# Optimization experiments

Measured on AMD Instinct MI355X. Metric: run time of the kernel, lower is better.

## Reference

```python
import jax, jax.numpy as jnp
import numpy as np

N, E, B, F, H = 100000, 800000, 128, 128, 128
G = 5
INV_BN = np.float32(1.0 / np.sqrt(1.0 + 1e-5))  # eval BatchNorm, running_mean=0, running_var=1

_HEAD_SHAPES = [("norm_emb_g", (2*H,)), ("norm_emb_b", (2*H,)),
                ("fc1_W", (16, 2*H+1)), ("fc1_b", (16,)),
                ("bn1_g", (16,)), ("bn1_b", (16,)),
                ("fc2_W", (2, 2*H+3)), ("fc2_b", (2,)),
                ("fc3a_W", (4, 2*H+5)), ("fc3a_b", (4,)),
                ("fc3b_W", (5, 2*H+5)), ("fc3b_b", (5,)),
                ("normc_g", (2*H+5,)), ("normc_b", (2*H+5,))]


def setup_inputs() -> dict:
    key = jax.random.key(0)
    ks = jax.random.split(key, 64)
    p = lambda i, shape: jax.random.normal(ks[i], shape, jnp.float32) * 0.05
    inp = {
        "x": jax.random.normal(ks[0], (N, F), jnp.float32),
        "edge_index": jax.random.randint(ks[1], (2, E), 0, N, dtype=jnp.int32),
        "edge_direction": jax.random.randint(ks[2], (E,), 0, 2, dtype=jnp.int32),
        "batch": jnp.sort(jax.random.randint(ks[3], (N,), 0, B, dtype=jnp.int32)),
        "graph_feature": jax.random.normal(ks[4], (B, G), jnp.float32),
        "task": 1,
    }
    i = 5
    for pref in ("pre", "suc"):
        for l in range(3):
            inp[pref + "_Wl%d" % l] = p(i, (H, H)); i += 1
            inp[pref + "_bl%d" % l] = p(i, (H,)); i += 1
            inp[pref + "_Wr%d" % l] = p(i, (H, H)); i += 1
    for name, shape in _HEAD_SHAPES:
        inp[name] = p(i, shape); i += 1
    return inp


def reference(x, edge_index, edge_direction, batch, graph_feature, task,
              pre_Wl0, pre_bl0, pre_Wr0, pre_Wl1, pre_bl1, pre_Wr1, pre_Wl2, pre_bl2, pre_Wr2,
              suc_Wl0, suc_bl0, suc_Wr0, suc_Wl1, suc_bl1, suc_Wr1, suc_Wl2, suc_bl2, suc_Wr2,
              norm_emb_g, norm_emb_b, fc1_W, fc1_b, bn1_g, bn1_b, fc2_W, fc2_b,
              fc3a_W, fc3a_b, fc3b_W, fc3b_b, normc_g, normc_b):
    src, dst = edge_index[0], edge_index[1]
    pre_mask = (edge_direction == 0).astype(x.dtype)
    suc_mask = (edge_direction == 1).astype(x.dtype)

    def sage(h, mask, Wl, bl, Wr):
        # PyG SAGEConv: lin_l(scatter_mean(x[src] -> dst)) + lin_r(h); masked edges emulate
        # the edge_direction slicing without data-dependent shapes.
        msg = h[src] * mask[:, None]                              # [E, H]
        agg = jax.ops.segment_sum(msg, dst, num_segments=N)      # [N, H]
        cnt = jax.ops.segment_sum(mask, dst, num_segments=N)     # [N]
        mean = agg / jnp.maximum(cnt, 1.0)[:, None]
        return mean @ Wl.T + bl + h @ Wr.T

    bn = lambda v, g, b: g * (v * INV_BN) + b  # eval-mode BatchNorm1d after reset

    pre_x, suc_x = x, x
    for Wl, bl, Wr in ((pre_Wl0, pre_bl0, pre_Wr0), (pre_Wl1, pre_bl1, pre_Wr1), (pre_Wl2, pre_bl2, pre_Wr2)):
        pre_x = jax.nn.relu(sage(pre_x, pre_mask, Wl, bl, Wr))
    for Wl, bl, Wr in ((suc_Wl0, suc_bl0, suc_Wr0), (suc_Wl1, suc_bl1, suc_Wr1), (suc_Wl2, suc_bl2, suc_Wr2)):
        suc_x = jax.nn.relu(sage(suc_x, suc_mask, Wl, bl, Wr))

    comb = jnp.concatenate([pre_x, suc_x], axis=1)               # [N, 2H]
    gsum = jax.ops.segment_sum(comb, batch, num_segments=B)
    gcnt = jax.ops.segment_sum(jnp.ones((N,), comb.dtype), batch, num_segments=B)
    combined = bn(gsum / jnp.maximum(gcnt, 1.0)[:, None], norm_emb_g, norm_emb_b)  # [B, 2H]

    lev_lsb = graph_feature[:, -1:]
    nx3 = graph_feature[:, -3:]
    out1 = bn(jax.nn.relu(jnp.concatenate([combined, lev_lsb], 1) @ fc1_W.T + fc1_b), bn1_g, bn1_b)
    out2 = jax.nn.relu(jnp.concatenate([combined, nx3], 1) @ fc2_W.T + fc2_b)
    pred = jnp.argmax(out2, axis=1)

    wf1 = graph_feature[:, 2:3]
    wf2 = graph_feature[:, 1:2]
    x3 = bn(jnp.concatenate([combined, wf1, wf2, nx3], 1), normc_g, normc_b)
    b1 = x3 @ fc3a_W.T + fc3a_b                                  # [B, 4]
    b2 = x3 @ fc3b_W.T + fc3b_b                                  # [B, 5]
    out3 = jnp.concatenate([jnp.where((pred == 0)[:, None], b1, 0.0),
                            jnp.where((pred == 1)[:, None], b2, 0.0)], axis=1)  # [B, 9]
    return (out1, out2, out3)
```

## Files before the change

kernel.cpp:

```cpp
#include <hip/hip_runtime.h>

constexpr int kN = 100000;
constexpr int kNpad = 100096;
constexpr int kE = 800000;
constexpr int kB = 128;
constexpr int kBinsPerDir = 391;
constexpr int kNB = 782;
constexpr int kRep = 64;
constexpr int kCtrs = kNB * kRep;
constexpr int kTiles = kNpad / 256;
constexpr float kInvBN = 0.99999500003749968f;

constexpr int kXconvBlocks = kNpad * 128 / 4 / 256;
constexpr int kWprepBlocks = 768;
constexpr int kBincountBlocks = (kE + 255) / 256;
constexpr int kGstartBlocks = (kN + 255) / 256;
constexpr int kPrepBlocks = kXconvBlocks + kWprepBlocks + kBincountBlocks + kGstartBlocks;

typedef short s16x8 __attribute__((ext_vector_type(8)));
typedef float f32x4 __attribute__((ext_vector_type(4)));

__device__ inline ushort bf16rne(float f) {
  uint u = __builtin_bit_cast(uint, f);
  u += 0x7fffu + ((u >> 16) & 1u);
  return (ushort)(u >> 16);
}
__device__ inline float bflo(uint v) { return __builtin_bit_cast(float, v << 16); }
__device__ inline float bfhi(uint v) { return __builtin_bit_cast(float, v & 0xffff0000u); }
__device__ inline uint pack2(float a, float b) {
  return (uint)bf16rne(a) | ((uint)bf16rne(b) << 16);
}

struct WPtrs { const float* Wl[6]; const float* Wr[6]; };


__global__ __launch_bounds__(256) void prep_kernel(
    const float* __restrict__ x, ushort* __restrict__ xb,
    WPtrs p, ushort* __restrict__ Wb,
    const int* __restrict__ ei, const int* __restrict__ ed,
    int* __restrict__ bincnt,
    const int* __restrict__ batch, int* __restrict__ gstart) {
  int bi = blockIdx.x;
  int t = threadIdx.x;
  if (bi < kXconvBlocks) {
    int i4 = (bi * 256 + t) * 4;
    ushort4 r;
    if (i4 < kN * 128) {
      float4 v = *(const float4*)&x[i4];
      r.x = bf16rne(v.x); r.y = bf16rne(v.y); r.z = bf16rne(v.z); r.w = bf16rne(v.w);
    } else {
      r.x = r.y = r.z = r.w = 0;
    }
    *(ushort4*)&xb[i4] = r;
  } else if (bi < kXconvBlocks + kWprepBlocks) {
    int id = (bi - kXconvBlocks) * 256 + t;
    int L = id >> 15;
    int o = (id >> 8) & 127, k = id & 255;
    const float* src = (k < 128) ? p.Wl[L] : p.Wr[L];
    Wb[id] = bf16rne(src[o * 128 + (k & 127)]);
  } else if (bi < kXconvBlocks + kWprepBlocks + kBincountBlocks) {
    int e = (bi - kXconvBlocks - kWprepBlocks) * 256 + t;
    if (e < kE) {
      int dst = ei[kE + e];
      int ctr = ((ed[e] * kBinsPerDir + (dst >> 8)) << 6) | ((e >> 8) & 63);
      atomicAdd(&bincnt[ctr], 1);
    }
  } else {
    int n = (bi - kXconvBlocks - kWprepBlocks - kBincountBlocks) * 256 + t;
    if (n < kN) {
      int b = batch[n];
      int bprev = (n == 0) ? -1 : batch[n - 1];
      for (int g = bprev + 1; g <= b; ++g) gstart[g] = n;
      if (n == kN - 1)
        for (int g = b + 1; g <= kB; ++g) gstart[g] = kN;
    }
  }
}


__global__ __launch_bounds__(256) void scan1_kernel(const int* __restrict__ in,
                                                    int* __restrict__ out,
                                                    int* __restrict__ bsum, int M) {
  __shared__ int s[256];
  int t = threadIdx.x;
  int idx = blockIdx.x * 1024 + t * 4;
  int4 v = {0, 0, 0, 0};
  if (idx < M) v = *(const int4*)&in[idx];
  int tsum = v.x + v.y + v.z + v.w;
  s[t] = tsum;
  __syncthreads();
  for (int d = 1; d < 256; d <<= 1) {
    int tmp = (t >= d) ? s[t - d] : 0;
    __syncthreads();
    s[t] += tmp;
    __syncthreads();
  }
  int excl = s[t] - tsum;
  if (idx < M) {
    int4 o;
    o.x = excl; o.y = excl + v.x; o.z = o.y + v.y; o.w = o.z + v.z;
    *(int4*)&out[idx] = o;
  }
  if (t == 255) bsum[blockIdx.x] = s[255];
}

__global__ __launch_bounds__(256) void scan2_kernel(int* __restrict__ bsum, int nb,
                                                    int* __restrict__ ghist) {
  __shared__ int s[256];
  int t = threadIdx.x;
  if (t < 128) ghist[t] = 0;
  int v = (t < nb) ? bsum[t] : 0;
  s[t] = v;
  __syncthreads();
  for (int d = 1; d < 256; d <<= 1) {
    int tmp = (t >= d) ? s[t - d] : 0;
    __syncthreads();
    s[t] += tmp;
    __syncthreads();
  }
  if (t < nb) bsum[t] = s[t] - v;
}

__global__ __launch_bounds__(256) void scan3_kernel(int* __restrict__ out,
                                                    const int* __restrict__ bsum, int M,
                                                    int* __restrict__ bincur) {
  int idx = blockIdx.x * 1024 + threadIdx.x * 4;
  int add = bsum[blockIdx.x];
  if (idx < M) {
    int4 o = *(int4*)&out[idx];
    o.x += add; o.y += add; o.z += add; o.w += add;
    *(int4*)&out[idx] = o;
    int4 z = {0, 0, 0, 0};
    *(int4*)&bincur[idx] = z;
  }
}


__global__ __launch_bounds__(256) void binscatter_kernel(const int* __restrict__ ei,
                                                         const int* __restrict__ ed,
                                                         const int* __restrict__ binoff,
                                                         int* __restrict__ bincur,
                                                         uint* __restrict__ binbuf,
                                                         float* __restrict__ comb_raw) {
  int gid = blockIdx.x * 256 + threadIdx.x;
  if (gid < kB * 256 / 4) {
    float4 z = {0.f, 0.f, 0.f, 0.f};
    *(float4*)&comb_raw[gid * 4] = z;
  }
  if (gid >= kE) return;
  int dst = ei[kE + gid];
  int ctr = ((ed[gid] * kBinsPerDir + (dst >> 8)) << 6) | ((gid >> 8) & 63);
  int pos = atomicAdd(&bincur[ctr], 1);
  binbuf[binoff[ctr] + pos] = (uint)ei[gid] | ((uint)(dst & 255) << 17);
}

__global__ __launch_bounds__(256) void binfill_kernel(const uint* __restrict__ binbuf,
                                                      const int* __restrict__ binoff,
                                                      int* __restrict__ csr,
                                                      int* __restrict__ cnt,
                                                      int* __restrict__ off,
                                                      int* __restrict__ ghist,
                                                      int* __restrict__ blockbase,
                                                      uint* __restrict__ perm) {
  __shared__ int lcnt[256];
  __shared__ int ls[256];
  __shared__ int lpos[256];
  int b = blockIdx.x;
  int t = threadIdx.x;
  perm[b * 256 + t] = (uint)kN;
  int dir = (b >= kBinsPerDir) ? 1 : 0;
  int nodeBase = (b - dir * kBinsPerDir) << 8;
  int e0 = binoff[b * kRep];
  int e1 = (b == kNB - 1) ? kE : binoff[(b + 1) * kRep];
  lcnt[t] = 0;
  __syncthreads();
  for (int e = e0 + t; e < e1; e += 256) atomicAdd(&lcnt[binbuf[e] >> 17], 1);
  __syncthreads();
  int my = lcnt[t];
  ls[t] = my;
  __syncthreads();
  for (int d = 1; d < 256; d <<= 1) {
    int tmp = (t >= d) ? ls[t - d] : 0;
    __syncthreads();
    ls[t] += tmp;
    __syncthreads();
  }
  int excl = ls[t] - my;
  lpos[t] = e0 + excl;
  int node = nodeBase + t;
  if (node < kN) {
    int g = dir * kN + node;
    cnt[g] = my;
    off[g] = e0 + excl;
  }
  if (t < 64) lcnt[t] = 0;
  __syncthreads();
  if (node < kN) atomicAdd(&lcnt[min(my, 63)], 1);
  __syncthreads();
  if (t < 64) blockbase[b * 64 + t] = atomicAdd(&ghist[dir * 64 + t], lcnt[t]);
  __syncthreads();
  for (int e = e0 + t; e < e1; e += 256) {
    uint v = binbuf[e];
    int pos = atomicAdd(&lpos[v >> 17], 1);
    csr[pos] = (int)(v & 0x1FFFFu);
  }
}


__global__ __launch_bounds__(64) void dscan_kernel(int* __restrict__ ghist) {
  __shared__ int s[64];
  int t = threadIdx.x;
  for (int dir = 0; dir < 2; ++dir) {
    int v = ghist[dir * 64 + t];
    s[t] = v;
    __syncthreads();
    for (int d = 1; d < 64; d <<= 1) {
      int tmp = (t >= d) ? s[t - d] : 0;
      __syncthreads();
      s[t] += tmp;
      __syncthreads();
    }
    ghist[dir * 64 + t] = s[t] - v;
    __syncthreads();
  }
}

__global__ __launch_bounds__(256) void dscatter_kernel(const int* __restrict__ cnt,
                                                       const int* __restrict__ ghist,
                                                       const int* __restrict__ blockbase,
                                                       uint* __restrict__ perm) {
  __shared__ int h[64];
  int b = blockIdx.x;
  int t = threadIdx.x;
  int dir = (b >= kBinsPerDir) ? 1 : 0;
  int node = (b - dir * kBinsPerDir) * 256 + t;
  if (t < 64) h[t] = 0;
  __syncthreads();
  if (node < kN) {
    int bucket = min(cnt[dir * kN + node], 63);
    int r = atomicAdd(&h[bucket], 1);
    int pos = ghist[dir * 64 + bucket] + blockbase[b * 64 + bucket] + r;
    int ch = pos >> 4, wi = pos & 15;
    int q = ch / 391, rr = ch - q * 391;
    int pos2 = ((rr * 16 + q) << 4) | wi;
    perm[dir * kNpad + pos2] = (uint)node;
  }
}


__global__ __launch_bounds__(1024) void fused_layer_kernel(
    const ushort* __restrict__ hin0, const ushort* __restrict__ hin1,
    ushort* __restrict__ hout0, ushort* __restrict__ hout1,
    const ushort* __restrict__ Wb0, const ushort* __restrict__ Wb1,
    const float* __restrict__ bl0, const float* __restrict__ bl1,
    const int* __restrict__ off, const int* __restrict__ cnt,
    const int* __restrict__ csr, const uint* __restrict__ perm) {
  __shared__ ushort Wlds[128 * 256];

  const int dir = (blockIdx.x >= kTiles) ? 1 : 0;
  const int tile = blockIdx.x - dir * kTiles;
  const ushort* __restrict__ h = dir ? hin1 : hin0;
  ushort* __restrict__ outp = dir ? hout1 : hout0;
  const ushort* __restrict__ Wb = dir ? Wb1 : Wb0;
  const float* __restrict__ bl = dir ? bl1 : bl0;
  const uint* __restrict__ pp = perm + (size_t)dir * kNpad;
  const int dirbase = dir * kN;

  const int t = threadIdx.x;
  const int w = t >> 6;
  const int l = t & 63;
  const int lr = l & 15;
  const int lq = l >> 4;
  const int swz = lr & 7;

  const int node = (int)pp[tile * 256 + w * 16 + lr];
  int s = 0, c = 0;
  if (node < kN) {
    int bkt = dirbase + node;
    s = off[bkt];
    c = cnt[bkt];
  }
  s16x8 self[4];
#pragma unroll
  for (int q = 0; q < 4; ++q)
    self[q] = *(const s16x8*)(h + (size_t)node * 128 + q * 32 + lq * 8);

#pragma unroll
  for (int it = 0; it < 4; ++it) {
    int u = t + 1024 * it;
    int o = u >> 5, b = u & 31;
    uint4 v = *(const uint4*)(Wb + (size_t)u * 8);
    *(uint4*)((char*)Wlds + o * 512 + ((b ^ (o & 7)) << 4)) = v;
  }
  __syncthreads();

  float ga[32];
#pragma unroll
  for (int i = 0; i < 32; ++i) ga[i] = 0.f;
  {
    const ushort* hp = h + lq * 8;
    int e = 0;
    for (; e + 2 <= c; e += 2) {
      int s0 = csr[s + e];
      int s1 = csr[s + e + 1];
      const ushort* p0 = hp + (size_t)s0 * 128;
      const ushort* p1 = hp + (size_t)s1 * 128;
      uint4 va[4], vb[4];
#pragma unroll
      for (int q = 0; q < 4; ++q) va[q] = *(const uint4*)(p0 + q * 32);
#pragma unroll
      for (int q = 0; q < 4; ++q) vb[q] = *(const uint4*)(p1 + q * 32);
#pragma unroll
      for (int q = 0; q < 4; ++q) {
        ga[q * 8 + 0] += bflo(va[q].x) + bflo(vb[q].x);
        ga[q * 8 + 1] += bfhi(va[q].x) + bfhi(vb[q].x);
        ga[q * 8 + 2] += bflo(va[q].y) + bflo(vb[q].y);
        ga[q * 8 + 3] += bfhi(va[q].y) + bfhi(vb[q].y);
        ga[q * 8 + 4] += bflo(va[q].z) + bflo(vb[q].z);
        ga[q * 8 + 5] += bfhi(va[q].z) + bfhi(vb[q].z);
        ga[q * 8 + 6] += bflo(va[q].w) + bflo(vb[q].w);
        ga[q * 8 + 7] += bfhi(va[q].w) + bfhi(vb[q].w);
      }
    }
    if (e < c) {
      int s0 = csr[s + e];
      const ushort* p0 = hp + (size_t)s0 * 128;
      uint4 va[4];
#pragma unroll
      for (int q = 0; q < 4; ++q) va[q] = *(const uint4*)(p0 + q * 32);
#pragma unroll
      for (int q = 0; q < 4; ++q) {
        ga[q * 8 + 0] += bflo(va[q].x);
        ga[q * 8 + 1] += bfhi(va[q].x);
        ga[q * 8 + 2] += bflo(va[q].y);
        ga[q * 8 + 3] += bfhi(va[q].y);
        ga[q * 8 + 4] += bflo(va[q].z);
        ga[q * 8 + 5] += bfhi(va[q].z);
        ga[q * 8 + 6] += bflo(va[q].w);
        ga[q * 8 + 7] += bfhi(va[q].w);
      }
    }
  }
  float iv = 1.0f / fmaxf((float)c, 1.0f);
  s16x8 am[4];
#pragma unroll
  for (int q = 0; q < 4; ++q) {
    uint4 r;
    r.x = pack2(ga[q * 8 + 0] * iv, ga[q * 8 + 1] * iv);
    r.y = pack2(ga[q * 8 + 2] * iv, ga[q * 8 + 3] * iv);
    r.z = pack2(ga[q * 8 + 4] * iv, ga[q * 8 + 5] * iv);
    r.w = pack2(ga[q * 8 + 6] * iv, ga[q * 8 + 7] * iv);
    am[q] = __builtin_bit_cast(s16x8, r);
  }

  f32x4 acc[8];
#pragma unroll
  for (int j = 0; j < 8; ++j) acc[j] = {0.f, 0.f, 0.f, 0.f};

#pragma unroll
  for (int kk = 0; kk < 8; ++kk) {
    s16x8 a = (kk < 4) ? am[kk] : self[kk - 4];
    const int ks = (kk * 4 + lq) ^ swz;
#pragma unroll
    for (int j = 0; j < 8; ++j) {
      int o = j * 16 + lr;
      s16x8 wf = *(const s16x8*)((const char*)Wlds + o * 512 + (ks << 4));
      acc[j] = __builtin_amdgcn_mfma_f32_16x16x32_bf16(wf, a, acc[j], 0, 0, 0);
    }
  }

  if (node < kN) {
#pragma unroll
    for (int j = 0; j < 8; ++j) {
      int o = j * 16 + lq * 4;
      float4 bv = *(const float4*)(bl + o);
      ushort4 r;
      r.x = bf16rne(fmaxf(acc[j][0] + bv.x, 0.f));
      r.y = bf16rne(fmaxf(acc[j][1] + bv.y, 0.f));
      r.z = bf16rne(fmaxf(acc[j][2] + bv.z, 0.f));
      r.w = bf16rne(fmaxf(acc[j][3] + bv.w, 0.f));
      *(ushort4*)(outp + (size_t)node * 128 + o) = r;
    }
  }
}


__global__ __launch_bounds__(256) void pool_kernel(const ushort* __restrict__ hp0,
                                                   const ushort* __restrict__ hp1,
                                                   const int* __restrict__ gstart,
                                                   float* __restrict__ comb_raw) {
  __shared__ float part[4 * 128];
  int gb = blockIdx.x;
  int dir = gb >> 11;
  int rem = gb & 2047;
  int graph = rem >> 4;
  int chunk = rem & 15;
  const ushort* __restrict__ h = dir ? hp1 : hp0;
  int base = dir << 7;
  int t = threadIdx.x;
  int slice = t >> 6;
  int col = t & 63;
  int s = gstart[graph];
  int e = gstart[graph + 1];
  int len = e - s;
  int c0 = s + (int)((long long)len * chunk / 16);
  int c1 = s + (int)((long long)len * (chunk + 1) / 16);
  float ax = 0.f, ay = 0.f;
  for (int n = c0 + slice; n < c1; n += 4) {
    uint v = *(const uint*)(h + (size_t)n * 128 + col * 2);
    ax += bflo(v);
    ay += bfhi(v);
  }
  part[slice * 128 + col * 2] = ax;
  part[slice * 128 + col * 2 + 1] = ay;
  __syncthreads();
  if (t < 128) {
    float v = part[t] + part[128 + t] + part[256 + t] + part[384 + t];
    atomicAdd(&comb_raw[graph * 256 + base + t], v);
  }
}


__global__ __launch_bounds__(256) void head_kernel(
    const float* __restrict__ comb_raw, const int* __restrict__ gstart,
    const float* __restrict__ gf,
    const float* __restrict__ neg, const float* __restrict__ neb,
    const float* __restrict__ fc1W, const float* __restrict__ fc1b,
    const float* __restrict__ bn1g, const float* __restrict__ bn1b,
    const float* __restrict__ fc2W, const float* __restrict__ fc2b,
    const float* __restrict__ fc3aW, const float* __restrict__ fc3ab,
    const float* __restrict__ fc3bW, const float* __restrict__ fc3bb,
    const float* __restrict__ ncg, const float* __restrict__ ncb,
    float* __restrict__ out) {
  __shared__ float wlds[6979];
  __shared__ float comb[256];
  __shared__ float x3[261];
  __shared__ float r2s[2];

  const int b = blockIdx.x;
  const int t = threadIdx.x;

  for (int i = t; i < 4112; i += 256) wlds[i] = fc1W[i];
  for (int i = t; i < 518; i += 256) wlds[4112 + i] = fc2W[i];
  for (int i = t; i < 1044; i += 256) wlds[4630 + i] = fc3aW[i];
  for (int i = t; i < 1305; i += 256) wlds[5674 + i] = fc3bW[i];

  float cntf = fmaxf((float)(gstart[b + 1] - gstart[b]), 1.0f);
  if (t < 256) comb[t] = neg[t] * ((comb_raw[b * 256 + t] / cntf) * kInvBN) + neb[t];
  __syncthreads();

  float g1 = gf[b * 5 + 1], g2 = gf[b * 5 + 2], g3 = gf[b * 5 + 3], g4 = gf[b * 5 + 4];
  const int g = t >> 3, l8 = t & 7;

  {
    float p = 0.f;
    if (g < 16) {
      const float* w = &wlds[g * 257];
      for (int j = l8; j < 256; j += 8) p += comb[j] * w[j];
    } else if (g < 18) {
      const float* w = &wlds[4112 + (g - 16) * 259];
      for (int j = l8; j < 256; j += 8) p += comb[j] * w[j];
    }
    p += __shfl_xor(p, 1);
    p += __shfl_xor(p, 2);
    p += __shfl_xor(p, 4);
    if (l8 == 0) {
      if (g < 16) {
        float z = fmaxf(p + wlds[g * 257 + 256] * g4 + fc1b[g], 0.f);
        out[b * 16 + g] = bn1g[g] * (z * kInvBN) + bn1b[g];
      } else if (g < 18) {
        int o = g - 16;
        const float* w = &wlds[4112 + o * 259];
        float z = fmaxf(p + w[256] * g2 + w[257] * g3 + w[258] * g4 + fc2b[o], 0.f);
        out[2048 + b * 2 + o] = z;
        r2s[o] = z;
      }
    }
  }
  for (int j = t; j < 261; j += 256) {
    float v;
    if (j < 256) v = comb[j];
    else if (j == 256) v = g2;
    else if (j == 257) v = g1;
    else if (j == 258) v = g2;
    else if (j == 259) v = g3;
    else v = g4;
    x3[j] = ncg[j] * (v * kInvBN) + ncb[j];
  }
  __syncthreads();
  int pred = (r2s[1] > r2s[0]) ? 1 : 0;

  {
    float p = 0.f;
    if (g < 4) {
      const float* w = &wlds[4630 + g * 261];
      for (int j = l8; j < 261; j += 8) p += x3[j] * w[j];
    } else if (g < 9) {
      const float* w = &wlds[5674 + (g - 4) * 261];
      for (int j = l8; j < 261; j += 8) p += x3[j] * w[j];
    }
    p += __shfl_xor(p, 1);
    p += __shfl_xor(p, 2);
    p += __shfl_xor(p, 4);
    if (l8 == 0) {
      if (g < 4) {
        float v = p + fc3ab[g];
        out[2304 + b * 9 + g] = (pred == 0) ? v : 0.f;
      } else if (g < 9) {
        int o = g - 4;
        float v = p + fc3bb[o];
        out[2304 + b * 9 + 4 + o] = (pred == 1) ? v : 0.f;
      }
    }
  }
}


extern "C" void kernel_launch(void* const* d_in, const int* in_sizes, int n_in,
                              void* d_out, int out_size, void* d_ws, size_t ws_size,
                              hipStream_t stream) {
  (void)in_sizes; (void)n_in; (void)out_size; (void)ws_size;
  const float* x   = (const float*)d_in[0];
  const int* ei    = (const int*)d_in[1];
  const int* ed    = (const int*)d_in[2];
  const int* batch = (const int*)d_in[3];
  const float* gf  = (const float*)d_in[4];

  char* ws = (char*)d_ws;
  auto carve = [&](size_t bytes) -> void* {
    void* p = ws;
    ws += (bytes + 255) & ~(size_t)255;
    return p;
  };
  int* cnt        = (int*)carve(2 * kN * sizeof(int));
  int* off        = (int*)carve(2 * kN * sizeof(int));
  int* bincnt     = (int*)carve(kCtrs * sizeof(int));
  int* bincur     = (int*)carve((kCtrs + 4) * sizeof(int));
  int* binoff     = (int*)carve((kCtrs + 4) * sizeof(int));
  int* bsum       = (int*)carve(1024);
  int* gstart     = (int*)carve((kB + 1) * sizeof(int));
  int* ghist      = (int*)carve(128 * sizeof(int));
  int* blockbase  = (int*)carve(kNB * 64 * sizeof(int));
  uint* perm      = (uint*)carve(2 * kNpad * sizeof(uint));
  int* csr        = (int*)carve(kE * sizeof(int));
  uint* binbuf    = (uint*)carve(kE * sizeof(uint));
  float* comb_raw = (float*)carve(kB * 256 * sizeof(float));
  ushort* xb      = (ushort*)carve((size_t)kNpad * 128 * 2);
  ushort* p0      = (ushort*)carve((size_t)kNpad * 128 * 2);
  ushort* p1      = (ushort*)carve((size_t)kNpad * 128 * 2);
  ushort* s0      = (ushort*)carve((size_t)kNpad * 128 * 2);
  ushort* Wb      = (ushort*)carve(6 * 128 * 256 * 2);

  hipMemsetAsync(bincnt, 0, kCtrs * sizeof(int), stream);

  WPtrs wp;
  for (int L = 0; L < 6; ++L) {
    wp.Wl[L] = (const float*)d_in[6 + 3 * L];
    wp.Wr[L] = (const float*)d_in[6 + 3 * L + 2];
  }

  prep_kernel<<<kPrepBlocks, 256, 0, stream>>>(x, xb, wp, Wb, ei, ed, bincnt, batch, gstart);

  constexpr int NBScan = (kCtrs + 1023) / 1024;
  scan1_kernel<<<NBScan, 256, 0, stream>>>(bincnt, binoff, bsum, kCtrs);
  scan2_kernel<<<1, 256, 0, stream>>>(bsum, NBScan, ghist);
  scan3_kernel<<<NBScan, 256, 0, stream>>>(binoff, bsum, kCtrs, bincur);
  binscatter_kernel<<<(kE + 255) / 256, 256, 0, stream>>>(ei, ed, binoff, bincur, binbuf, comb_raw);
  binfill_kernel<<<kNB, 256, 0, stream>>>(binbuf, binoff, csr, cnt, off, ghist, blockbase, perm);
  dscan_kernel<<<1, 64, 0, stream>>>(ghist);
  dscatter_kernel<<<kNB, 256, 0, stream>>>(cnt, ghist, blockbase, perm);

  auto W = [&](int L) { return Wb + (size_t)L * 32768; };
  auto B = [&](int L) { return (const float*)d_in[6 + 3 * L + 1]; };

  fused_layer_kernel<<<2 * kTiles, 1024, 0, stream>>>(
      xb, xb, p0, s0, W(0), W(3), B(0), B(3), off, cnt, csr, perm);
  fused_layer_kernel<<<2 * kTiles, 1024, 0, stream>>>(
      p0, s0, p1, xb, W(1), W(4), B(1), B(4), off, cnt, csr, perm);
  fused_layer_kernel<<<2 * kTiles, 1024, 0, stream>>>(
      p1, xb, p0, s0, W(2), W(5), B(2), B(5), off, cnt, csr, perm);

  pool_kernel<<<2 * kB * 16, 256, 0, stream>>>(p0, s0, gstart, comb_raw);

  head_kernel<<<kB, 256, 0, stream>>>(
      comb_raw, gstart, gf,
      (const float*)d_in[24], (const float*)d_in[25],
      (const float*)d_in[26], (const float*)d_in[27],
      (const float*)d_in[28], (const float*)d_in[29],
      (const float*)d_in[30], (const float*)d_in[31],
      (const float*)d_in[32], (const float*)d_in[33],
      (const float*)d_in[34], (const float*)d_in[35],
      (const float*)d_in[36], (const float*)d_in[37],
      (float*)d_out);
}
```

Before: 362.5 us.

## Vectorize prep stages and unroll neighbor gather by four

The prep kernel now converts x with grid-stride loops over 8 elements per thread. It also converts weights with float4 loads and bins edges four per thread using int4 loads, which shrinks the block counts. The SAGE aggregation loop is unrolled to four neighbor rows per iteration instead of two, putting more independent gather loads in flight to hide memory latency. The cost is higher register pressure in the aggregation kernel, which may lower occupancy.

```diff
diff --git a/kernel.cpp b/kernel.cpp
--- a/kernel.cpp
+++ b/kernel.cpp
@@ -11,10 +11,10 @@
 constexpr int kTiles = kNpad / 256;
 constexpr float kInvBN = 0.99999500003749968f;
 
-constexpr int kXconvBlocks = kNpad * 128 / 4 / 256;
-constexpr int kWprepBlocks = 768;
-constexpr int kBincountBlocks = (kE + 255) / 256;
-constexpr int kGstartBlocks = (kN + 255) / 256;
+constexpr int kXconvBlocks = 1024;
+constexpr int kWprepBlocks = 192;
+constexpr int kBincountBlocks = 782;
+constexpr int kGstartBlocks = 391;
 constexpr int kPrepBlocks = kXconvBlocks + kWprepBlocks + kBincountBlocks + kGstartBlocks;
 
 typedef short s16x8 __attribute__((ext_vector_type(8)));
@@ -43,27 +43,47 @@
   int bi = blockIdx.x;
   int t = threadIdx.x;
   if (bi < kXconvBlocks) {
-    int i4 = (bi * 256 + t) * 4;
+    constexpr int total = kNpad * 128 / 8;
+    constexpr int stride = kXconvBlocks * 256;
+    for (int i = bi * 256 + t; i < total; i += stride) {
+      int i8 = i * 8;
+      ushort4 r0, r1;
+      if (i8 < kN * 128) {
+        float4 v0 = *(const float4*)&x[i8];
+        float4 v1 = *(const float4*)&x[i8 + 4];
+        r0.x = bf16rne(v0.x); r0.y = bf16rne(v0.y); r0.z = bf16rne(v0.z); r0.w = bf16rne(v0.w);
+        r1.x = bf16rne(v1.x); r1.y = bf16rne(v1.y); r1.z = bf16rne(v1.z); r1.w = bf16rne(v1.w);
+      } else {
+        r0.x = r0.y = r0.z = r0.w = 0;
+        r1 = r0;
+      }
+      *(ushort4*)&xb[i8] = r0;
+      *(ushort4*)&xb[i8 + 4] = r1;
+    }
+  } else if (bi < kXconvBlocks + kWprepBlocks) {
+    int id4 = ((bi - kXconvBlocks) * 256 + t) * 4;
+    int L = id4 >> 15;
+    int o = (id4 >> 8) & 127, k = id4 & 255;
+    const float* src = (k < 128) ? p.Wl[L] : p.Wr[L];
+    float4 v = *(const float4*)&src[o * 128 + (k & 127)];
     ushort4 r;
-    if (i4 < kN * 128) {
-      float4 v = *(const float4*)&x[i4];
-      r.x = bf16rne(v.x); r.y = bf16rne(v.y); r.z = bf16rne(v.z); r.w = bf16rne(v.w);
-    } else {
-      r.x = r.y = r.z = r.w = 0;
-    }
-    *(ushort4*)&xb[i4] = r;
-  } else if (bi < kXconvBlocks + kWprepBlocks) {
-    int id = (bi - kXconvBlocks) * 256 + t;
-    int L = id >> 15;
-    int o = (id >> 8) & 127, k = id & 255;
-    const float* src = (k < 128) ? p.Wl[L] : p.Wr[L];
-    Wb[id] = bf16rne(src[o * 128 + (k & 127)]);
+    r.x = bf16rne(v.x); r.y = bf16rne(v.y); r.z = bf16rne(v.z); r.w = bf16rne(v.w);
+    *(ushort4*)&Wb[id4] = r;
   } else if (bi < kXconvBlocks + kWprepBlocks + kBincountBlocks) {
-    int e = (bi - kXconvBlocks - kWprepBlocks) * 256 + t;
-    if (e < kE) {
-      int dst = ei[kE + e];
-      int ctr = ((ed[e] * kBinsPerDir + (dst >> 8)) << 6) | ((e >> 8) & 63);
-      atomicAdd(&bincnt[ctr], 1);
+    int e4 = ((bi - kXconvBlocks - kWprepBlocks) * 256 + t) * 4;
+    if (e4 < kE) {
+      int4 dv = *(const int4*)&ed[e4];
+      int4 sv = *(const int4*)&ei[kE + e4];
+      int dsts[4] = {sv.x, sv.y, sv.z, sv.w};
+      int dirs[4] = {dv.x, dv.y, dv.z, dv.w};
+#pragma unroll
+      for (int k = 0; k < 4; ++k) {
+        int e = e4 + k;
+        if (e < kE) {
+          int ctr = ((dirs[k] * kBinsPerDir + (dsts[k] >> 8)) << 6) | ((e >> 8) & 63);
+          atomicAdd(&bincnt[ctr], 1);
+        }
+      }
     }
   } else {
     int n = (bi - kXconvBlocks - kWprepBlocks - kBincountBlocks) * 256 + t;
@@ -299,46 +319,52 @@
   for (int i = 0; i < 32; ++i) ga[i] = 0.f;
   {
     const ushort* hp = h + lq * 8;
+    auto acc1 = [&](const uint4* v) {
+#pragma unroll
+      for (int q = 0; q < 4; ++q) {
+        ga[q * 8 + 0] += bflo(v[q].x); ga[q * 8 + 1] += bfhi(v[q].x);
+        ga[q * 8 + 2] += bflo(v[q].y); ga[q * 8 + 3] += bfhi(v[q].y);
+        ga[q * 8 + 4] += bflo(v[q].z); ga[q * 8 + 5] += bfhi(v[q].z);
+        ga[q * 8 + 6] += bflo(v[q].w); ga[q * 8 + 7] += bfhi(v[q].w);
+      }
+    };
     int e = 0;
-    for (; e + 2 <= c; e += 2) {
-      int s0 = csr[s + e];
-      int s1 = csr[s + e + 1];
-      const ushort* p0 = hp + (size_t)s0 * 128;
-      const ushort* p1 = hp + (size_t)s1 * 128;
-      uint4 va[4], vb[4];
-#pragma unroll
-      for (int q = 0; q < 4; ++q) va[q] = *(const uint4*)(p0 + q * 32);
-#pragma unroll
-      for (int q = 0; q < 4; ++q) vb[q] = *(const uint4*)(p1 + q * 32);
-#pragma unroll
-      for (int q = 0; q < 4; ++q) {
-        ga[q * 8 + 0] += bflo(va[q].x) + bflo(vb[q].x);
-        ga[q * 8 + 1] += bfhi(va[q].x) + bfhi(vb[q].x);
-        ga[q * 8 + 2] += bflo(va[q].y) + bflo(vb[q].y);
-        ga[q * 8 + 3] += bfhi(va[q].y) + bfhi(vb[q].y);
-        ga[q * 8 + 4] += bflo(va[q].z) + bflo(vb[q].z);
-        ga[q * 8 + 5] += bfhi(va[q].z) + bfhi(vb[q].z);
-        ga[q * 8 + 6] += bflo(va[q].w) + bflo(vb[q].w);
-        ga[q * 8 + 7] += bfhi(va[q].w) + bfhi(vb[q].w);
-      }
+    for (; e + 4 <= c; e += 4) {
+      int s0 = csr[s + e], s1 = csr[s + e + 1], s2 = csr[s + e + 2], s3 = csr[s + e + 3];
+      const ushort* q0 = hp + (size_t)s0 * 128;
+      const ushort* q1 = hp + (size_t)s1 * 128;
+      const ushort* q2 = hp + (size_t)s2 * 128;
+      const ushort* q3 = hp + (size_t)s3 * 128;
+      uint4 v0[4], v1[4], v2[4], v3[4];
+#pragma unroll
+      for (int q = 0; q < 4; ++q) v0[q] = *(const uint4*)(q0 + q * 32);
+#pragma unroll
+      for (int q = 0; q < 4; ++q) v1[q] = *(const uint4*)(q1 + q * 32);
+#pragma unroll
+      for (int q = 0; q < 4; ++q) v2[q] = *(const uint4*)(q2 + q * 32);
+#pragma unroll
+      for (int q = 0; q < 4; ++q) v3[q] = *(const uint4*)(q3 + q * 32);
+      acc1(v0); acc1(v1); acc1(v2); acc1(v3);
+    }
+    if (e + 2 <= c) {
+      int s0 = csr[s + e], s1 = csr[s + e + 1];
+      const ushort* q0 = hp + (size_t)s0 * 128;
+      const ushort* q1 = hp + (size_t)s1 * 128;
+      uint4 v0[4], v1[4];
+#pragma unroll
+      for (int q = 0; q < 4; ++q) v0[q] = *(const uint4*)(q0 + q * 32);
+#pragma unroll
+      for (int q = 0; q < 4; ++q) v1[q] = *(const uint4*)(q1 + q * 32);
+      acc1(v0); acc1(v1);
+      e += 2;
     }
     if (e < c) {
       int s0 = csr[s + e];
-      const ushort* p0 = hp + (size_t)s0 * 128;
-      uint4 va[4];
-#pragma unroll
-      for (int q = 0; q < 4; ++q) va[q] = *(const uint4*)(p0 + q * 32);
-#pragma unroll
-      for (int q = 0; q < 4; ++q) {
-        ga[q * 8 + 0] += bflo(va[q].x);
-        ga[q * 8 + 1] += bfhi(va[q].x);
-        ga[q * 8 + 2] += bflo(va[q].y);
-        ga[q * 8 + 3] += bfhi(va[q].y);
-        ga[q * 8 + 4] += bflo(va[q].z);
-        ga[q * 8 + 5] += bfhi(va[q].z);
-        ga[q * 8 + 6] += bflo(va[q].w);
-        ga[q * 8 + 7] += bfhi(va[q].w);
-      }
+      const ushort* q0 = hp + (size_t)s0 * 128;
+      uint4 v0[4];
+#pragma unroll
+      for (int q = 0; q < 4; ++q) v0[q] = *(const uint4*)(q0 + q * 32);
+      acc1(v0);
     }
   }
   float iv = 1.0f / fmaxf((float)c, 1.0f);
```

Result: slower. 460.8 us (+27.1%).
